# Kernel optimization log

Hardware: AMD Instinct MI355X
Metric: run time of the kernel (lower is better)

Reference implementation:

```python
import jax, jax.numpy as jnp
import numpy as np

SIGMA = 1.0
EPS = 1e-8  # torch nn.CosineSimilarity eps


def setup_inputs() -> dict:
    key = jax.random.key(0)
    kx, ky = jax.random.split(key)
    ex = jax.random.normal(kx, (8192, 768), dtype=jnp.float32)
    ey = jax.random.normal(ky, (16384, 768), dtype=jnp.float32)
    return {"ex": ex, "ey": ey}


def _halfnormal_log_prob(v, sigma):
    # HalfNormal(sigma).log_prob(v) = 0.5*log(2/pi) - log(sigma) - v^2/(2 sigma^2)
    logc = 0.5 * jnp.log(jnp.asarray(2.0 / np.pi, v.dtype)) - jnp.log(jnp.asarray(sigma, v.dtype))
    return logc - v * v / (2.0 * sigma * sigma)


def reference(ex, ey):
    Nx, Ny = ex.shape[0], ey.shape[0]
    # cosine similarity matrix [Nx, Ny]; norms clamped like torch CosineSimilarity
    nx = jnp.maximum(jnp.linalg.norm(ex, axis=-1), EPS)  # [Nx]
    ny = jnp.maximum(jnp.linalg.norm(ey, axis=-1), EPS)  # [Ny]
    sims = jnp.einsum('nd,md->nm', ex, ey) / (nx[:, None] * ny[None, :])
    # dim = argmax([Nx, Ny]); Nx < Ny here -> reduce over axis 1 (ey side)
    dim = int(np.argmax([Nx, Ny]))
    C = sims.max(axis=dim)  # length min(Nx, Ny)
    x = 1.0 - C[:Nx]
    y = 1.0 - C[:Ny]
    lx = _halfnormal_log_prob(x, SIGMA)
    ly = _halfnormal_log_prob(y, SIGMA)
    return ((-jnp.exp(lx) * lx).sum(), (-jnp.exp(ly) * ly).sum())
```

## Files before the change

kernel.cpp:

```cpp
#include <hip/hip_runtime.h>
#include <hip/hip_bf16.h>
#include <cstdint>

#define D_DIM 768
#define BM 128
#define BN 256
#define BK 128

typedef int   intx8    __attribute__((ext_vector_type(8)));
typedef float floatx16 __attribute__((ext_vector_type(16)));

#define SCALE_ONE 0x7F7F7F7F


__device__ inline void lds_load16(const void* g, void* lds) {
  __builtin_amdgcn_global_load_lds(
      (const __attribute__((address_space(1))) unsigned int*)g,
      (__attribute__((address_space(3))) unsigned int*)lds,
      16, 0, 0);
}

__device__ inline intx8 ldfrag(const unsigned char* p, int o0, int o1) {
  intx8 r;
  *(int4*)&r       = *(const int4*)(p + o0);
  *((int4*)&r + 1) = *(const int4*)(p + o1);
  return r;
}


__global__ __launch_bounds__(256) void norm_cast_kernel(
    const float* __restrict__ EX, const float* __restrict__ EY,
    unsigned int* __restrict__ XO, unsigned int* __restrict__ YO, int Nx) {
  int row = blockIdx.x * 4 + (threadIdx.x >> 6);
  int lane = threadIdx.x & 63;
  const float* X = (row < Nx) ? EX : EY;
  unsigned int* Y = (row < Nx) ? XO : YO;
  int r = (row < Nx) ? row : (row - Nx);
  const float4* xr = (const float4*)(X + (size_t)r * D_DIM);
  float4 a = xr[lane];
  float4 b = xr[lane + 64];
  float4 c = xr[lane + 128];
  float ss = a.x*a.x + a.y*a.y + a.z*a.z + a.w*a.w
           + b.x*b.x + b.y*b.y + b.z*b.z + b.w*b.w
           + c.x*c.x + c.y*c.y + c.z*c.z + c.w*c.w;
  #pragma unroll
  for (int off = 32; off > 0; off >>= 1) ss += __shfl_xor(ss, off, 64);
  float s = 1.0f / fmaxf(sqrtf(ss), 1e-8f);
  unsigned int* yr = Y + (size_t)r * (D_DIM / 4);
  int d;
  d = __builtin_amdgcn_cvt_pk_fp8_f32(a.x * s, a.y * s, 0, false);
  d = __builtin_amdgcn_cvt_pk_fp8_f32(a.z * s, a.w * s, d, true);
  yr[lane] = (unsigned int)d;
  d = __builtin_amdgcn_cvt_pk_fp8_f32(b.x * s, b.y * s, 0, false);
  d = __builtin_amdgcn_cvt_pk_fp8_f32(b.z * s, b.w * s, d, true);
  yr[lane + 64] = (unsigned int)d;
  d = __builtin_amdgcn_cvt_pk_fp8_f32(c.x * s, c.y * s, 0, false);
  d = __builtin_amdgcn_cvt_pk_fp8_f32(c.z * s, c.w * s, d, true);
  yr[lane + 128] = (unsigned int)d;
}


__global__ __launch_bounds__(256, 2) void gemm_max_kernel(
    const unsigned char* __restrict__ A,
    const unsigned char* __restrict__ B,
    float* __restrict__ partial,
    int Nx) {
  __shared__ unsigned char As[BM * BK];
  __shared__ unsigned char Bs[BN * BK];
  __shared__ float red[2][BM];

  const int tid  = threadIdx.x;
  const int wave = tid >> 6;
  const int lane = tid & 63;
  const int wm = wave >> 1;
  const int wn = wave & 1;
  const int l31 = lane & 31;
  const int h   = lane >> 5;
  const int skey = l31 & 7;

  const int bm0 = blockIdx.x * BM;
  const int bn0 = blockIdx.y * BN;

  floatx16 acc[2][4];
  #pragma unroll
  for (int mt = 0; mt < 2; ++mt)
    #pragma unroll
    for (int nt = 0; nt < 4; ++nt)
      acc[mt][nt] = (floatx16)(0.f);

  const unsigned char* pA0 = As + (size_t)(wm * 64 + 0  + l31) * BK;
  const unsigned char* pA1 = As + (size_t)(wm * 64 + 32 + l31) * BK;
  const unsigned char* pB0 = Bs + (size_t)(wn * 128 + 0   + l31) * BK;
  const unsigned char* pB1 = Bs + (size_t)(wn * 128 + 32  + l31) * BK;
  const unsigned char* pB2 = Bs + (size_t)(wn * 128 + 64  + l31) * BK;
  const unsigned char* pB3 = Bs + (size_t)(wn * 128 + 96  + l31) * BK;

  const int srow = lane >> 3;
  const int sj = (lane & 7) ^ (srow & 7);
  const unsigned char* gA = A + (size_t)(bm0 + wave * 32 + srow) * D_DIM + sj * 16;
  const unsigned char* gB = B + (size_t)(bn0 + wave * 64 + srow) * D_DIM + sj * 16;
  unsigned char* lA0 = As + (size_t)(wave * 32) * BK;
  unsigned char* lB0 = Bs + (size_t)(wave * 64) * BK;
  const size_t g8 = (size_t)8 * D_DIM;

  for (int k0 = 0; k0 < D_DIM; k0 += BK) {
    __syncthreads();
    #pragma unroll
    for (int i = 0; i < 4; ++i)
      lds_load16(gA + k0 + i * g8, lA0 + i * 1024);
    #pragma unroll
    for (int i = 0; i < 8; ++i)
      lds_load16(gB + k0 + i * g8, lB0 + i * 1024);
    __syncthreads();

    #pragma unroll
    for (int ks = 0; ks < 2; ++ks) {
      const int c0 = ks * 4 + 2 * h;
      const int o0 = (c0 ^ skey) * 16;
      const int o1 = ((c0 + 1) ^ skey) * 16;
      intx8 a0 = ldfrag(pA0, o0, o1);
      intx8 a1 = ldfrag(pA1, o0, o1);
      intx8 b;
      b = ldfrag(pB0, o0, o1);
      acc[0][0] = __builtin_amdgcn_mfma_scale_f32_32x32x64_f8f6f4(
          a0, b, acc[0][0], 0, 0, 0, SCALE_ONE, 0, SCALE_ONE);
      acc[1][0] = __builtin_amdgcn_mfma_scale_f32_32x32x64_f8f6f4(
          a1, b, acc[1][0], 0, 0, 0, SCALE_ONE, 0, SCALE_ONE);
      b = ldfrag(pB1, o0, o1);
      acc[0][1] = __builtin_amdgcn_mfma_scale_f32_32x32x64_f8f6f4(
          a0, b, acc[0][1], 0, 0, 0, SCALE_ONE, 0, SCALE_ONE);
      acc[1][1] = __builtin_amdgcn_mfma_scale_f32_32x32x64_f8f6f4(
          a1, b, acc[1][1], 0, 0, 0, SCALE_ONE, 0, SCALE_ONE);
      b = ldfrag(pB2, o0, o1);
      acc[0][2] = __builtin_amdgcn_mfma_scale_f32_32x32x64_f8f6f4(
          a0, b, acc[0][2], 0, 0, 0, SCALE_ONE, 0, SCALE_ONE);
      acc[1][2] = __builtin_amdgcn_mfma_scale_f32_32x32x64_f8f6f4(
          a1, b, acc[1][2], 0, 0, 0, SCALE_ONE, 0, SCALE_ONE);
      b = ldfrag(pB3, o0, o1);
      acc[0][3] = __builtin_amdgcn_mfma_scale_f32_32x32x64_f8f6f4(
          a0, b, acc[0][3], 0, 0, 0, SCALE_ONE, 0, SCALE_ONE);
      acc[1][3] = __builtin_amdgcn_mfma_scale_f32_32x32x64_f8f6f4(
          a1, b, acc[1][3], 0, 0, 0, SCALE_ONE, 0, SCALE_ONE);
    }
  }

  #pragma unroll
  for (int mt = 0; mt < 2; ++mt) {
    #pragma unroll
    for (int reg = 0; reg < 16; ++reg) {
      float v = fmaxf(fmaxf(acc[mt][0][reg], acc[mt][1][reg]),
                      fmaxf(acc[mt][2][reg], acc[mt][3][reg]));
      #pragma unroll
      for (int off = 1; off < 32; off <<= 1)
        v = fmaxf(v, __shfl_xor(v, off, 64));
      if (l31 == 0) {
        int r = wm * 64 + mt * 32 + (reg & 3) + 8 * (reg >> 2) + 4 * h;
        red[wn][r] = v;
      }
    }
  }
  __syncthreads();
  if (tid < BM) {
    float m = fmaxf(red[0][tid], red[1][tid]);
    partial[(size_t)blockIdx.y * Nx + bm0 + tid] = m;
  }
}


__global__ __launch_bounds__(256) void rowmax_kernel(
    const float* __restrict__ partial, float* __restrict__ bsum, int Nx, int ncb) {
  __shared__ float sdata[4];
  int r = blockIdx.x * blockDim.x + threadIdx.x;
  float m = -1e30f;
  for (int cb = 0; cb < ncb; ++cb)
    m = fmaxf(m, partial[(size_t)cb * Nx + r]);
  float x = 1.0f - m;
  const float logc = -0.22579135264472744f;
  float l = logc - 0.5f * x * x;
  float t = -__expf(l) * l;
  #pragma unroll
  for (int off = 32; off > 0; off >>= 1) t += __shfl_xor(t, off, 64);
  int wave = threadIdx.x >> 6;
  int lane = threadIdx.x & 63;
  if (lane == 0) sdata[wave] = t;
  __syncthreads();
  if (threadIdx.x == 0)
    bsum[blockIdx.x] = sdata[0] + sdata[1] + sdata[2] + sdata[3];
}


__global__ __launch_bounds__(64) void final_kernel(
    const float* __restrict__ bsum, float* __restrict__ out, int nb) {
  int lane = threadIdx.x;
  float s = (lane < nb) ? bsum[lane] : 0.f;
  #pragma unroll
  for (int off = 32; off > 0; off >>= 1) s += __shfl_xor(s, off, 64);
  if (lane == 0) { out[0] = s; out[1] = s; }
}


extern "C" void kernel_launch(void* const* d_in, const int* in_sizes, int n_in,
                              void* d_out, int out_size, void* d_ws, size_t ws_size,
                              hipStream_t stream) {
  const float* ex = (const float*)d_in[0];
  const float* ey = (const float*)d_in[1];
  const int Nx = in_sizes[0] / D_DIM;
  const int Ny = in_sizes[1] / D_DIM;
  const int ncb = Ny / BN;

  char* ws = (char*)d_ws;
  unsigned char* exn = (unsigned char*)ws;
  unsigned char* eyn = exn + (size_t)Nx * D_DIM;
  float* partial = (float*)(ws + (size_t)(Nx + Ny) * D_DIM);
  float* bsum    = partial + (size_t)ncb * Nx;

  norm_cast_kernel<<<(Nx + Ny) / 4, 256, 0, stream>>>(
      ex, ey, (unsigned int*)exn, (unsigned int*)eyn, Nx);
  gemm_max_kernel<<<dim3(Nx / BM, Ny / BN), 256, 0, stream>>>(exn, eyn, partial, Nx);
  rowmax_kernel<<<Nx / 256, 256, 0, stream>>>(partial, bsum, Nx, ncb);
  final_kernel<<<1, 64, 0, stream>>>(bsum, (float*)d_out, Nx / 256);
}
```

Before: 251.4 us.

## Pre-swizzle A into MFMA fragment layout, load from global, double-buffer B

The normalize/cast kernel now writes the fp8 ex matrix in a blocked layout that matches the MFMA A-fragment order, 32 rows per block. The GEMM then loads A fragments straight from global memory into registers and no longer stages A through LDS. B tiles are double-buffered in LDS, with the next K tile prefetched while the current one is computed, which halves the barriers per iteration. The cost is more global traffic for A per block, since A fragments are re-read through cache instead of shared across waves in LDS, and extra memory latency sits on the MFMA critical path.

```diff
diff --git a/kernel.cpp b/kernel.cpp
--- a/kernel.cpp
+++ b/kernel.cpp
@@ -6,6 +6,8 @@
 #define BM 128
 #define BN 256
 #define BK 128
+#define KCH (D_DIM / 64)
+#define RBLK 24576
 
 typedef int   intx8    __attribute__((ext_vector_type(8)));
 typedef float floatx16 __attribute__((ext_vector_type(16)));
@@ -20,7 +22,7 @@
       16, 0, 0);
 }
 
-__device__ inline intx8 ldfrag(const unsigned char* p, int o0, int o1) {
+__device__ inline intx8 ldfrag2(const unsigned char* p, int o0, int o1) {
   intx8 r;
   *(int4*)&r       = *(const int4*)(p + o0);
   *((int4*)&r + 1) = *(const int4*)(p + o1);
@@ -33,9 +35,9 @@
     unsigned int* __restrict__ XO, unsigned int* __restrict__ YO, int Nx) {
   int row = blockIdx.x * 4 + (threadIdx.x >> 6);
   int lane = threadIdx.x & 63;
-  const float* X = (row < Nx) ? EX : EY;
-  unsigned int* Y = (row < Nx) ? XO : YO;
-  int r = (row < Nx) ? row : (row - Nx);
+  bool isA = row < Nx;
+  const float* X = isA ? EX : EY;
+  int r = isA ? row : (row - Nx);
   const float4* xr = (const float4*)(X + (size_t)r * D_DIM);
   float4 a = xr[lane];
   float4 b = xr[lane + 64];
@@ -46,17 +48,26 @@
   #pragma unroll
   for (int off = 32; off > 0; off >>= 1) ss += __shfl_xor(ss, off, 64);
   float s = 1.0f / fmaxf(sqrtf(ss), 1e-8f);
-  unsigned int* yr = Y + (size_t)r * (D_DIM / 4);
-  int d;
-  d = __builtin_amdgcn_cvt_pk_fp8_f32(a.x * s, a.y * s, 0, false);
-  d = __builtin_amdgcn_cvt_pk_fp8_f32(a.z * s, a.w * s, d, true);
-  yr[lane] = (unsigned int)d;
-  d = __builtin_amdgcn_cvt_pk_fp8_f32(b.x * s, b.y * s, 0, false);
-  d = __builtin_amdgcn_cvt_pk_fp8_f32(b.z * s, b.w * s, d, true);
-  yr[lane + 64] = (unsigned int)d;
-  d = __builtin_amdgcn_cvt_pk_fp8_f32(c.x * s, c.y * s, 0, false);
-  d = __builtin_amdgcn_cvt_pk_fp8_f32(c.z * s, c.w * s, d, true);
-  yr[lane + 128] = (unsigned int)d;
+  int d0, d1, d2;
+  d0 = __builtin_amdgcn_cvt_pk_fp8_f32(a.x * s, a.y * s, 0, false);
+  d0 = __builtin_amdgcn_cvt_pk_fp8_f32(a.z * s, a.w * s, d0, true);
+  d1 = __builtin_amdgcn_cvt_pk_fp8_f32(b.x * s, b.y * s, 0, false);
+  d1 = __builtin_amdgcn_cvt_pk_fp8_f32(b.z * s, b.w * s, d1, true);
+  d2 = __builtin_amdgcn_cvt_pk_fp8_f32(c.x * s, c.y * s, 0, false);
+  d2 = __builtin_amdgcn_cvt_pk_fp8_f32(c.z * s, c.w * s, d2, true);
+  if (isA) {
+    unsigned int* dst = (unsigned int*)((char*)XO + (size_t)(r >> 5) * RBLK);
+    int off = ((lane >> 4) * 2048) + (((lane >> 2) & 1) * 1024)
+            + ((((lane >> 3) & 1) * 32 + (r & 31)) * 16) + ((lane & 3) * 4);
+    dst[off >> 2]           = (unsigned int)d0;
+    dst[(off + 8192) >> 2]  = (unsigned int)d1;
+    dst[(off + 16384) >> 2] = (unsigned int)d2;
+  } else {
+    unsigned int* yr = YO + (size_t)r * (D_DIM / 4);
+    yr[lane]       = (unsigned int)d0;
+    yr[lane + 64]  = (unsigned int)d1;
+    yr[lane + 128] = (unsigned int)d2;
+  }
 }
 
 
@@ -65,8 +76,7 @@
     const unsigned char* __restrict__ B,
     float* __restrict__ partial,
     int Nx) {
-  __shared__ unsigned char As[BM * BK];
-  __shared__ unsigned char Bs[BN * BK];
+  __shared__ unsigned char Bs[2][BN * BK];
   __shared__ float red[2][BM];
 
   const int tid  = threadIdx.x;
@@ -78,9 +88,6 @@
   const int h   = lane >> 5;
   const int skey = l31 & 7;
 
-  const int bm0 = blockIdx.x * BM;
-  const int bn0 = blockIdx.y * BN;
-
   floatx16 acc[2][4];
   #pragma unroll
   for (int mt = 0; mt < 2; ++mt)
@@ -88,60 +95,72 @@
     for (int nt = 0; nt < 4; ++nt)
       acc[mt][nt] = (floatx16)(0.f);
 
-  const unsigned char* pA0 = As + (size_t)(wm * 64 + 0  + l31) * BK;
-  const unsigned char* pA1 = As + (size_t)(wm * 64 + 32 + l31) * BK;
-  const unsigned char* pB0 = Bs + (size_t)(wn * 128 + 0   + l31) * BK;
-  const unsigned char* pB1 = Bs + (size_t)(wn * 128 + 32  + l31) * BK;
-  const unsigned char* pB2 = Bs + (size_t)(wn * 128 + 64  + l31) * BK;
-  const unsigned char* pB3 = Bs + (size_t)(wn * 128 + 96  + l31) * BK;
+  const unsigned char* aB[2];
+  #pragma unroll
+  for (int mt = 0; mt < 2; ++mt)
+    aB[mt] = A + (size_t)(blockIdx.x * 4 + wm * 2 + mt) * RBLK + lane * 16;
 
   const int srow = lane >> 3;
   const int sj = (lane & 7) ^ (srow & 7);
-  const unsigned char* gA = A + (size_t)(bm0 + wave * 32 + srow) * D_DIM + sj * 16;
-  const unsigned char* gB = B + (size_t)(bn0 + wave * 64 + srow) * D_DIM + sj * 16;
-  unsigned char* lA0 = As + (size_t)(wave * 32) * BK;
-  unsigned char* lB0 = Bs + (size_t)(wave * 64) * BK;
+  const unsigned char* gB =
+      B + (size_t)(blockIdx.y * BN + wave * 64 + srow) * D_DIM + sj * 16;
   const size_t g8 = (size_t)8 * D_DIM;
-
-  for (int k0 = 0; k0 < D_DIM; k0 += BK) {
-    __syncthreads();
-    #pragma unroll
-    for (int i = 0; i < 4; ++i)
-      lds_load16(gA + k0 + i * g8, lA0 + i * 1024);
-    #pragma unroll
-    for (int i = 0; i < 8; ++i)
-      lds_load16(gB + k0 + i * g8, lB0 + i * 1024);
-    __syncthreads();
-
+  unsigned char* lB[2] = { Bs[0] + (size_t)(wave * 64) * BK,
+                           Bs[1] + (size_t)(wave * 64) * BK };
+
+  const unsigned char* pB[2][4];
+  #pragma unroll
+  for (int bufi = 0; bufi < 2; ++bufi)
+    #pragma unroll
+    for (int nt = 0; nt < 4; ++nt)
+      pB[bufi][nt] = Bs[bufi] + (size_t)(wn * 128 + nt * 32 + l31) * BK;
+
+  #pragma unroll
+  for (int i = 0; i < 8; ++i)
+    lds_load16(gB + i * g8, lB[0] + i * 1024);
+  __syncthreads();
+
+  #pragma unroll
+  for (int kt = 0; kt < D_DIM / BK; ++kt) {
+    const int cur = kt & 1;
+    if (kt + 1 < D_DIM / BK) {
+      #pragma unroll
+      for (int i = 0; i < 8; ++i)
+        lds_load16(gB + (kt + 1) * BK + i * g8, lB[cur ^ 1] + i * 1024);
+    }
     #pragma unroll
     for (int ks = 0; ks < 2; ++ks) {
+      const int kc = kt * 2 + ks;
       const int c0 = ks * 4 + 2 * h;
       const int o0 = (c0 ^ skey) * 16;
       const int o1 = ((c0 + 1) ^ skey) * 16;
-      intx8 a0 = ldfrag(pA0, o0, o1);
-      intx8 a1 = ldfrag(pA1, o0, o1);
-      intx8 b;
-      b = ldfrag(pB0, o0, o1);
+      intx8 a0, a1, b;
+      { const unsigned char* p = aB[0] + kc * 2048;
+        *(int4*)&a0 = *(const int4*)p; *((int4*)&a0 + 1) = *(const int4*)(p + 1024); }
+      { const unsigned char* p = aB[1] + kc * 2048;
+        *(int4*)&a1 = *(const int4*)p; *((int4*)&a1 + 1) = *(const int4*)(p + 1024); }
+      b = ldfrag2(pB[cur][0], o0, o1);
       acc[0][0] = __builtin_amdgcn_mfma_scale_f32_32x32x64_f8f6f4(
           a0, b, acc[0][0], 0, 0, 0, SCALE_ONE, 0, SCALE_ONE);
       acc[1][0] = __builtin_amdgcn_mfma_scale_f32_32x32x64_f8f6f4(
           a1, b, acc[1][0], 0, 0, 0, SCALE_ONE, 0, SCALE_ONE);
-      b = ldfrag(pB1, o0, o1);
+      b = ldfrag2(pB[cur][1], o0, o1);
       acc[0][1] = __builtin_amdgcn_mfma_scale_f32_32x32x64_f8f6f4(
           a0, b, acc[0][1], 0, 0, 0, SCALE_ONE, 0, SCALE_ONE);
       acc[1][1] = __builtin_amdgcn_mfma_scale_f32_32x32x64_f8f6f4(
           a1, b, acc[1][1], 0, 0, 0, SCALE_ONE, 0, SCALE_ONE);
-      b = ldfrag(pB2, o0, o1);
+      b = ldfrag2(pB[cur][2], o0, o1);
       acc[0][2] = __builtin_amdgcn_mfma_scale_f32_32x32x64_f8f6f4(
           a0, b, acc[0][2], 0, 0, 0, SCALE_ONE, 0, SCALE_ONE);
       acc[1][2] = __builtin_amdgcn_mfma_scale_f32_32x32x64_f8f6f4(
           a1, b, acc[1][2], 0, 0, 0, SCALE_ONE, 0, SCALE_ONE);
-      b = ldfrag(pB3, o0, o1);
+      b = ldfrag2(pB[cur][3], o0, o1);
       acc[0][3] = __builtin_amdgcn_mfma_scale_f32_32x32x64_f8f6f4(
           a0, b, acc[0][3], 0, 0, 0, SCALE_ONE, 0, SCALE_ONE);
       acc[1][3] = __builtin_amdgcn_mfma_scale_f32_32x32x64_f8f6f4(
           a1, b, acc[1][3], 0, 0, 0, SCALE_ONE, 0, SCALE_ONE);
     }
+    __syncthreads();
   }
 
   #pragma unroll
@@ -162,7 +181,7 @@
   __syncthreads();
   if (tid < BM) {
     float m = fmaxf(red[0][tid], red[1][tid]);
-    partial[(size_t)blockIdx.y * Nx + bm0 + tid] = m;
+    partial[(size_t)blockIdx.y * Nx + blockIdx.x * BM + tid] = m;
   }
 }
 
@@ -210,8 +229,8 @@
 
   char* ws = (char*)d_ws;
   unsigned char* exn = (unsigned char*)ws;
-  unsigned char* eyn = exn + (size_t)Nx * D_DIM;
-  float* partial = (float*)(ws + (size_t)(Nx + Ny) * D_DIM);
+  unsigned char* eyn = exn + (size_t)(Nx / 32) * RBLK;
+  float* partial = (float*)(eyn + (size_t)Ny * D_DIM);
   float* bsum    = partial + (size_t)ncb * Nx;
 
   norm_cast_kernel<<<(Nx + Ny) / 4, 256, 0, stream>>>(
```

After: 632.9 us. 152% more time.

## Double-buffer LDS tiles with a smaller K step to overlap loads and MFMA

Applied to the files above, without the earlier changes.

The GEMM main loop switches from single-buffered 128-wide K tiles to two 64-wide K-tile LDS buffers. The next tile's global-to-LDS DMA is issued before the MFMAs on the current tile, and only one barrier per iteration is kept. The XOR swizzle is dropped in favour of a simple contiguous 64-byte row layout with two 16-byte fragment reads per lane. This is meant to hide global load latency behind matrix math. In exchange it runs more, shorter iterations, and the unswizzled layout may raise LDS bank conflicts.

```diff
diff --git a/kernel.cpp b/kernel.cpp
--- a/kernel.cpp
+++ b/kernel.cpp
@@ -5,7 +5,8 @@
 #define D_DIM 768
 #define BM 128
 #define BN 256
-#define BK 128
+#define BK 64
+#define NKT (D_DIM / BK)
 
 typedef int   intx8    __attribute__((ext_vector_type(8)));
 typedef float floatx16 __attribute__((ext_vector_type(16)));
@@ -20,10 +21,10 @@
       16, 0, 0);
 }
 
-__device__ inline intx8 ldfrag(const unsigned char* p, int o0, int o1) {
+__device__ inline intx8 ldfrag32(const unsigned char* p) {
   intx8 r;
-  *(int4*)&r       = *(const int4*)(p + o0);
-  *((int4*)&r + 1) = *(const int4*)(p + o1);
+  *(int4*)&r       = *(const int4*)p;
+  *((int4*)&r + 1) = *(const int4*)(p + 16);
   return r;
 }
 
@@ -65,8 +66,8 @@
     const unsigned char* __restrict__ B,
     float* __restrict__ partial,
     int Nx) {
-  __shared__ unsigned char As[BM * BK];
-  __shared__ unsigned char Bs[BN * BK];
+  __shared__ unsigned char As[2 * BM * BK];
+  __shared__ unsigned char Bs[2 * BN * BK];
   __shared__ float red[2][BM];
 
   const int tid  = threadIdx.x;
@@ -76,10 +77,6 @@
   const int wn = wave & 1;
   const int l31 = lane & 31;
   const int h   = lane >> 5;
-  const int skey = l31 & 7;
-
-  const int bm0 = blockIdx.x * BM;
-  const int bn0 = blockIdx.y * BN;
 
   floatx16 acc[2][4];
   #pragma unroll
@@ -88,60 +85,67 @@
     for (int nt = 0; nt < 4; ++nt)
       acc[mt][nt] = (floatx16)(0.f);
 
-  const unsigned char* pA0 = As + (size_t)(wm * 64 + 0  + l31) * BK;
-  const unsigned char* pA1 = As + (size_t)(wm * 64 + 32 + l31) * BK;
-  const unsigned char* pB0 = Bs + (size_t)(wn * 128 + 0   + l31) * BK;
-  const unsigned char* pB1 = Bs + (size_t)(wn * 128 + 32  + l31) * BK;
-  const unsigned char* pB2 = Bs + (size_t)(wn * 128 + 64  + l31) * BK;
-  const unsigned char* pB3 = Bs + (size_t)(wn * 128 + 96  + l31) * BK;
-
-  const int srow = lane >> 3;
-  const int sj = (lane & 7) ^ (srow & 7);
-  const unsigned char* gA = A + (size_t)(bm0 + wave * 32 + srow) * D_DIM + sj * 16;
-  const unsigned char* gB = B + (size_t)(bn0 + wave * 64 + srow) * D_DIM + sj * 16;
-  unsigned char* lA0 = As + (size_t)(wave * 32) * BK;
-  unsigned char* lB0 = Bs + (size_t)(wave * 64) * BK;
-  const size_t g8 = (size_t)8 * D_DIM;
-
-  for (int k0 = 0; k0 < D_DIM; k0 += BK) {
+  const int srow = lane >> 2;
+  const int schk = (lane & 3) * 16;
+  const unsigned char* gA =
+      A + (size_t)(blockIdx.x * BM + wave * 32 + srow) * D_DIM + schk;
+  const unsigned char* gB =
+      B + (size_t)(blockIdx.y * BN + wave * 64 + srow) * D_DIM + schk;
+  const size_t g16 = (size_t)16 * D_DIM;
+  unsigned char* lA = As + (size_t)(wave * 32) * BK;
+  unsigned char* lB = Bs + (size_t)(wave * 64) * BK;
+
+  const unsigned char* pA0 = As + (size_t)(wm * 64 + 0  + l31) * BK + h * 32;
+  const unsigned char* pA1 = As + (size_t)(wm * 64 + 32 + l31) * BK + h * 32;
+  const unsigned char* pB0 = Bs + (size_t)(wn * 128 + 0  + l31) * BK + h * 32;
+  const unsigned char* pB1 = Bs + (size_t)(wn * 128 + 32 + l31) * BK + h * 32;
+  const unsigned char* pB2 = Bs + (size_t)(wn * 128 + 64 + l31) * BK + h * 32;
+  const unsigned char* pB3 = Bs + (size_t)(wn * 128 + 96 + l31) * BK + h * 32;
+
+  #pragma unroll
+  for (int i = 0; i < 2; ++i) lds_load16(gA + i * g16, lA + i * 1024);
+  #pragma unroll
+  for (int i = 0; i < 4; ++i) lds_load16(gB + i * g16, lB + i * 1024);
+  __syncthreads();
+
+  #pragma unroll
+  for (int kt = 0; kt < NKT; ++kt) {
+    const int cur = kt & 1;
+    if (kt + 1 < NKT) {
+      const int nb = cur ^ 1;
+      #pragma unroll
+      for (int i = 0; i < 2; ++i)
+        lds_load16(gA + (kt + 1) * BK + i * g16, lA + nb * (BM * BK) + i * 1024);
+      #pragma unroll
+      for (int i = 0; i < 4; ++i)
+        lds_load16(gB + (kt + 1) * BK + i * g16, lB + nb * (BN * BK) + i * 1024);
+    }
+    const int oA = cur * (BM * BK);
+    const int oB = cur * (BN * BK);
+    intx8 a0 = ldfrag32(pA0 + oA);
+    intx8 a1 = ldfrag32(pA1 + oA);
+    intx8 b;
+    b = ldfrag32(pB0 + oB);
+    acc[0][0] = __builtin_amdgcn_mfma_scale_f32_32x32x64_f8f6f4(
+        a0, b, acc[0][0], 0, 0, 0, SCALE_ONE, 0, SCALE_ONE);
+    acc[1][0] = __builtin_amdgcn_mfma_scale_f32_32x32x64_f8f6f4(
+        a1, b, acc[1][0], 0, 0, 0, SCALE_ONE, 0, SCALE_ONE);
+    b = ldfrag32(pB1 + oB);
+    acc[0][1] = __builtin_amdgcn_mfma_scale_f32_32x32x64_f8f6f4(
+        a0, b, acc[0][1], 0, 0, 0, SCALE_ONE, 0, SCALE_ONE);
+    acc[1][1] = __builtin_amdgcn_mfma_scale_f32_32x32x64_f8f6f4(
+        a1, b, acc[1][1], 0, 0, 0, SCALE_ONE, 0, SCALE_ONE);
+    b = ldfrag32(pB2 + oB);
+    acc[0][2] = __builtin_amdgcn_mfma_scale_f32_32x32x64_f8f6f4(
+        a0, b, acc[0][2], 0, 0, 0, SCALE_ONE, 0, SCALE_ONE);
+    acc[1][2] = __builtin_amdgcn_mfma_scale_f32_32x32x64_f8f6f4(
+        a1, b, acc[1][2], 0, 0, 0, SCALE_ONE, 0, SCALE_ONE);
+    b = ldfrag32(pB3 + oB);
+    acc[0][3] = __builtin_amdgcn_mfma_scale_f32_32x32x64_f8f6f4(
+        a0, b, acc[0][3], 0, 0, 0, SCALE_ONE, 0, SCALE_ONE);
+    acc[1][3] = __builtin_amdgcn_mfma_scale_f32_32x32x64_f8f6f4(
+        a1, b, acc[1][3], 0, 0, 0, SCALE_ONE, 0, SCALE_ONE);
     __syncthreads();
-    #pragma unroll
-    for (int i = 0; i < 4; ++i)
-      lds_load16(gA + k0 + i * g8, lA0 + i * 1024);
-    #pragma unroll
-    for (int i = 0; i < 8; ++i)
-      lds_load16(gB + k0 + i * g8, lB0 + i * 1024);
-    __syncthreads();
-
-    #pragma unroll
-    for (int ks = 0; ks < 2; ++ks) {
-      const int c0 = ks * 4 + 2 * h;
-      const int o0 = (c0 ^ skey) * 16;
-      const int o1 = ((c0 + 1) ^ skey) * 16;
-      intx8 a0 = ldfrag(pA0, o0, o1);
-      intx8 a1 = ldfrag(pA1, o0, o1);
-      intx8 b;
-      b = ldfrag(pB0, o0, o1);
-      acc[0][0] = __builtin_amdgcn_mfma_scale_f32_32x32x64_f8f6f4(
-          a0, b, acc[0][0], 0, 0, 0, SCALE_ONE, 0, SCALE_ONE);
-      acc[1][0] = __builtin_amdgcn_mfma_scale_f32_32x32x64_f8f6f4(
-          a1, b, acc[1][0], 0, 0, 0, SCALE_ONE, 0, SCALE_ONE);
-      b = ldfrag(pB1, o0, o1);
-      acc[0][1] = __builtin_amdgcn_mfma_scale_f32_32x32x64_f8f6f4(
-          a0, b, acc[0][1], 0, 0, 0, SCALE_ONE, 0, SCALE_ONE);
-      acc[1][1] = __builtin_amdgcn_mfma_scale_f32_32x32x64_f8f6f4(
-          a1, b, acc[1][1], 0, 0, 0, SCALE_ONE, 0, SCALE_ONE);
-      b = ldfrag(pB2, o0, o1);
-      acc[0][2] = __builtin_amdgcn_mfma_scale_f32_32x32x64_f8f6f4(
-          a0, b, acc[0][2], 0, 0, 0, SCALE_ONE, 0, SCALE_ONE);
-      acc[1][2] = __builtin_amdgcn_mfma_scale_f32_32x32x64_f8f6f4(
-          a1, b, acc[1][2], 0, 0, 0, SCALE_ONE, 0, SCALE_ONE);
-      b = ldfrag(pB3, o0, o1);
-      acc[0][3] = __builtin_amdgcn_mfma_scale_f32_32x32x64_f8f6f4(
-          a0, b, acc[0][3], 0, 0, 0, SCALE_ONE, 0, SCALE_ONE);
-      acc[1][3] = __builtin_amdgcn_mfma_scale_f32_32x32x64_f8f6f4(
-          a1, b, acc[1][3], 0, 0, 0, SCALE_ONE, 0, SCALE_ONE);
-    }
   }
 
   #pragma unroll
@@ -162,7 +166,7 @@
   __syncthreads();
   if (tid < BM) {
     float m = fmaxf(red[0][tid], red[1][tid]);
-    partial[(size_t)blockIdx.y * Nx + bm0 + tid] = m;
+    partial[(size_t)blockIdx.y * Nx + blockIdx.x * BM + tid] = m;
   }
 }
 
@@ -211,7 +215,7 @@
   char* ws = (char*)d_ws;
   unsigned char* exn = (unsigned char*)ws;
   unsigned char* eyn = exn + (size_t)Nx * D_DIM;
-  float* partial = (float*)(ws + (size_t)(Nx + Ny) * D_DIM);
+  float* partial = (float*)(eyn + (size_t)Ny * D_DIM);
   float* bsum    = partial + (size_t)ncb * Nx;
 
   norm_cast_kernel<<<(Nx + Ny) / 4, 256, 0, stream>>>(
```

New measurement: 644.7 us. 156% more time.
